# Performance work log

Hardware: AMD Instinct MI355X
Metric: run time of the kernel (lower is better)

Reference implementation:

```python
import jax, jax.numpy as jnp
import numpy as np

EPS = 1e-6

def _phi(x):
    # ELU + 1 feature map: strictly positive
    return jax.nn.elu(x) + 1.0

def setup_inputs() -> dict:
    key = jax.random.key(0)
    kq, kk, kv = jax.random.split(key, 3)
    B, T, H, D = 4, 8192, 16, 64
    q = jax.random.normal(kq, (B, T, H, D), dtype=jnp.float32)
    k = jax.random.normal(kk, (B, T, H, D), dtype=jnp.float32)
    v = jax.random.normal(kv, (B, T, H, D), dtype=jnp.float32)
    return {"q": q, "k": k, "v": v}

def _linear_attention(q, k, v):
    # q,k,v: [B,T,H,D] -> out [B,T,H,D]
    phi_q = _phi(q)
    phi_k = _phi(k)
    # time-major for scan: [T,B,H,D]
    pq = jnp.moveaxis(phi_q, 1, 0)
    pk = jnp.moveaxis(phi_k, 1, 0)
    vv = jnp.moveaxis(v, 1, 0)
    B, H, D = pq.shape[1], pq.shape[2], pq.shape[3]
    S0 = jnp.zeros((B, H, D, D), dtype=q.dtype)
    z0 = jnp.zeros((B, H, D), dtype=q.dtype)

    def step(carry, inp):
        S, z = carry
        q_t, k_t, v_t = inp  # each [B,H,D]
        S = S + k_t[..., :, None] * v_t[..., None, :]  # [B,H,D,D]
        z = z + k_t
        num = jnp.einsum('bhd,bhde->bhe', q_t, S)
        den = jnp.einsum('bhd,bhd->bh', q_t, z) + EPS
        return (S, z), num / den[..., None]

    _, out = jax.lax.scan(step, (S0, z0), (pq, pk, vv))
    return jnp.moveaxis(out, 0, 1)  # [B,T,H,D]

def reference(q, k, v):
    return _linear_attention(q, k, v)
```

## Files before the change

kernel.cpp:

```cpp
#include <hip/hip_runtime.h>
#include <hip/hip_bf16.h>


#define EPS_ 1e-6f

constexpr int Bc  = 4;
constexpr int Tc  = 8192;
constexpr int Hc  = 16;
constexpr int Dc  = 64;
constexpr int CH  = 128;
constexpr int NCH = Tc / CH;
constexpr int BHc = Bc * Hc;
constexpr int REC = Dc * Dc + Dc;
constexpr int SEG = 16;
constexpr int CPS = NCH / SEG;

typedef short  bf16x8 __attribute__((ext_vector_type(8)));
typedef float  f32x4  __attribute__((ext_vector_type(4)));

__device__ __forceinline__ float phi_f(float x) {
    return x > 0.f ? x + 1.f : __expf(x);
}
__device__ __forceinline__ unsigned short f2b(float x) {
    __hip_bfloat16 b = __float2bfloat16(x);
    return __builtin_bit_cast(unsigned short, b);
}
__device__ __forceinline__ float b2f(unsigned short u) {
    return __uint_as_float(((unsigned)u) << 16);
}

__global__ __launch_bounds__(256, 4) void k_chunkscan(const float* __restrict__ kin,
                                                      const float* __restrict__ vin,
                                                      float* __restrict__ ws) {
    const int blk = blockIdx.x;
    const int bh  = blk >> 4, seg = blk & (SEG - 1);
    const int b   = bh >> 4,  h   = bh & 15;
    const int tid = threadIdx.x;
    const int w = tid >> 6, lane = tid & 63;
    const int l15 = lane & 15, quad = lane >> 4;

    __shared__ unsigned short ktr[64][136];
    __shared__ unsigned short vtr[64][136];
    __shared__ float zred[16][64];

    const int c0 = (tid & 15) << 2;
    const int rl = (tid >> 4) << 2;

    f32x4 acc[4];
    #pragma unroll
    for (int nt = 0; nt < 4; nt++) acc[nt] = (f32x4){0.f, 0.f, 0.f, 0.f};
    float zrun = 0.f;

    for (int i = 0; i < CPS; ++i) {
        const int c  = seg * CPS + i;
        const int t0 = c * CH;

        unsigned short hk[2][4][4], hv[2][4][4];
        float zp[4] = {0.f, 0.f, 0.f, 0.f};
        #pragma unroll
        for (int sh = 0; sh < 2; ++sh) {
            const int r0 = rl + sh * 64;
            #pragma unroll
            for (int jj = 0; jj < 4; ++jj) {
                const size_t g = ((((size_t)b * Tc) + (t0 + r0 + jj)) * Hc + h) * Dc + c0;
                const float4 kk = *(const float4*)(kin + g);
                const float4 vv = *(const float4*)(vin + g);
                hk[sh][jj][0] = f2b(phi_f(kk.x)); hk[sh][jj][1] = f2b(phi_f(kk.y));
                hk[sh][jj][2] = f2b(phi_f(kk.z)); hk[sh][jj][3] = f2b(phi_f(kk.w));
                hv[sh][jj][0] = f2b(vv.x); hv[sh][jj][1] = f2b(vv.y);
                hv[sh][jj][2] = f2b(vv.z); hv[sh][jj][3] = f2b(vv.w);
                #pragma unroll
                for (int j = 0; j < 4; ++j) zp[j] += b2f(hk[sh][jj][j]);
            }
        }
        __syncthreads();

        #pragma unroll
        for (int sh = 0; sh < 2; ++sh) {
            const int r0 = rl + sh * 64;
            #pragma unroll
            for (int j = 0; j < 4; ++j) {
                *(ushort4*)&ktr[c0 + j][r0] =
                    make_ushort4(hk[sh][0][j], hk[sh][1][j], hk[sh][2][j], hk[sh][3][j]);
                *(ushort4*)&vtr[c0 + j][r0] =
                    make_ushort4(hv[sh][0][j], hv[sh][1][j], hv[sh][2][j], hv[sh][3][j]);
            }
        }
        #pragma unroll
        for (int j = 0; j < 4; ++j) zred[tid >> 4][c0 + j] = zp[j];

        float* rec = ws + (size_t)(bh * NCH + c) * REC;
        if (i > 0) {
            #pragma unroll
            for (int nt = 0; nt < 4; nt++)
                #pragma unroll
                for (int r = 0; r < 4; r++)
                    rec[(16 * w + quad * 4 + r) * 64 + 16 * nt + l15] = acc[nt][r];
        }
        __syncthreads();

        if (tid < 64) {
            if (i > 0) rec[4096 + tid] = zrun;
            float zs = 0.f;
            #pragma unroll
            for (int g = 0; g < 16; g++) zs += zred[g][tid];
            zrun += zs;
        }

        #pragma unroll
        for (int ks = 0; ks < 4; ks++) {
            bf16x8 a = *(const bf16x8*)&vtr[16 * w + l15][quad * 8 + ks * 32];
            #pragma unroll
            for (int nt = 0; nt < 4; nt++) {
                bf16x8 bb = *(const bf16x8*)&ktr[16 * nt + l15][quad * 8 + ks * 32];
                acc[nt] = __builtin_amdgcn_mfma_f32_16x16x32_bf16(a, bb, acc[nt], 0, 0, 0);
            }
        }
    }

    {
        float* rec0 = ws + (size_t)(bh * NCH + seg * CPS) * REC;
        #pragma unroll
        for (int nt = 0; nt < 4; nt++)
            #pragma unroll
            for (int r = 0; r < 4; r++)
                rec0[(16 * w + quad * 4 + r) * 64 + 16 * nt + l15] = acc[nt][r];
        if (tid < 64) rec0[4096 + tid] = zrun;
    }
}

__global__ __launch_bounds__(256) void k_segscan(float* __restrict__ ws) {
    const int bh = blockIdx.x;
    const int e  = blockIdx.y * 256 + threadIdx.x;
    if (e >= REC) return;
    float* p = ws + (size_t)bh * NCH * REC + e;
    float t[SEG];
    #pragma unroll
    for (int s = 0; s < SEG; ++s) t[s] = p[(size_t)(s * CPS) * REC];
    float run = 0.f;
    #pragma unroll
    for (int s = 0; s < SEG; ++s) { p[(size_t)(s * CPS) * REC] = run; run += t[s]; }
}

__global__ __launch_bounds__(512, 4) void k_output(const float* __restrict__ qin,
                                                   const float* __restrict__ kin,
                                                   const float* __restrict__ vin,
                                                   const float* __restrict__ ws,
                                                   float* __restrict__ outp) {
    const int chunk = blockIdx.x;
    const int bh = chunk >> 6, c = chunk & (NCH - 1);
    const int b = bh >> 4, h = bh & 15;
    const int t0 = c * CH;
    const int tid = threadIdx.x;
    const int w = tid >> 6, lane = tid & 63;
    const int l15 = lane & 15, quad = lane >> 4;

    __shared__ unsigned short qb[128][72];
    __shared__ unsigned short kb[128][72];
    __shared__ unsigned short sb[64][72];
    __shared__ unsigned short vb[64][136];
    __shared__ float zsh[64];
    __shared__ float den[128];

    {
        const int row = tid >> 2, cb = (tid & 3) << 4;
        const size_t g = ((((size_t)b * Tc) + (t0 + row)) * Hc + h) * Dc + cb;
        const float4* qp = (const float4*)(qin + g);
        const float4* kp = (const float4*)(kin + g);
        #pragma unroll
        for (int i = 0; i < 4; i++) {
            float4 qq = qp[i];
            float4 kk = kp[i];
            *(ushort4*)&qb[row][cb + 4 * i] =
                make_ushort4(f2b(phi_f(qq.x)), f2b(phi_f(qq.y)), f2b(phi_f(qq.z)), f2b(phi_f(qq.w)));
            *(ushort4*)&kb[row][cb + 4 * i] =
                make_ushort4(f2b(phi_f(kk.x)), f2b(phi_f(kk.y)), f2b(phi_f(kk.z)), f2b(phi_f(kk.w)));
        }
    }
    {
        const int c0 = (tid & 15) << 2;
        const int r0 = (tid >> 4) << 2;
        unsigned short hv[4][4];
        #pragma unroll
        for (int jj = 0; jj < 4; ++jj) {
            const size_t g = ((((size_t)b * Tc) + (t0 + r0 + jj)) * Hc + h) * Dc + c0;
            const float4 vv = *(const float4*)(vin + g);
            hv[jj][0] = f2b(vv.x); hv[jj][1] = f2b(vv.y);
            hv[jj][2] = f2b(vv.z); hv[jj][3] = f2b(vv.w);
        }
        #pragma unroll
        for (int j = 0; j < 4; ++j)
            *(ushort4*)&vb[c0 + j][r0] = make_ushort4(hv[0][j], hv[1][j], hv[2][j], hv[3][j]);
    }
    {
        const float* rec = ws + (size_t)chunk * REC;
        const float* bse = ws + (size_t)(bh * NCH + (c & ~(CPS - 1))) * REC;
        const bool cz = ((c & (CPS - 1)) == 0);
        #pragma unroll
        for (int i = 0; i < 2; i++) {
            const int idx = tid + i * 512;
            float4 sv = ((const float4*)rec)[idx];
            float4 bv = ((const float4*)bse)[idx];
            float4 t;
            if (cz) t = bv;
            else { t.x = sv.x + bv.x; t.y = sv.y + bv.y; t.z = sv.z + bv.z; t.w = sv.w + bv.w; }
            const int flat = idx * 4, e = flat >> 6, d = flat & 63;
            *(ushort4*)&sb[e][d] = make_ushort4(f2b(t.x), f2b(t.y), f2b(t.z), f2b(t.w));
        }
        if (tid < 16) {
            float4 zv = ((const float4*)(rec + 4096))[tid];
            float4 bz = ((const float4*)(bse + 4096))[tid];
            float4 t;
            if (cz) t = bz;
            else { t.x = zv.x + bz.x; t.y = zv.y + bz.y; t.z = zv.z + bz.z; t.w = zv.w + bz.w; }
            zsh[tid * 4 + 0] = t.x; zsh[tid * 4 + 1] = t.y;
            zsh[tid * 4 + 2] = t.z; zsh[tid * 4 + 3] = t.w;
        }
    }
    __syncthreads();

    if (tid < 128) {
        float s = 0.f;
        #pragma unroll
        for (int j = 0; j < 8; j++) {
            bf16x8 qv = *(const bf16x8*)&qb[tid][j * 8];
            #pragma unroll
            for (int u = 0; u < 8; u++) s += b2f((unsigned short)qv[u]) * zsh[j * 8 + u];
        }
        den[tid] = s + EPS_;
    }

    f32x4 acc[4];
    #pragma unroll
    for (int nt = 0; nt < 4; nt++) acc[nt] = (f32x4){0.f, 0.f, 0.f, 0.f};
    #pragma unroll
    for (int ks = 0; ks < 2; ks++) {
        bf16x8 a = *(const bf16x8*)&qb[16 * w + l15][quad * 8 + ks * 32];
        #pragma unroll
        for (int nt = 0; nt < 4; nt++) {
            bf16x8 bb = *(const bf16x8*)&sb[16 * nt + l15][quad * 8 + ks * 32];
            acc[nt] = __builtin_amdgcn_mfma_f32_16x16x32_bf16(a, bb, acc[nt], 0, 0, 0);
        }
    }

    f32x4 wt[8];
    #pragma unroll
    for (int nt = 0; nt < 8; nt++) wt[nt] = (f32x4){0.f, 0.f, 0.f, 0.f};
    #pragma unroll
    for (int ks = 0; ks < 2; ks++) {
        bf16x8 a = *(const bf16x8*)&qb[16 * w + l15][quad * 8 + ks * 32];
        #pragma unroll
        for (int nt = 0; nt < 4; nt++) {
            bf16x8 bb = *(const bf16x8*)&kb[16 * nt + l15][quad * 8 + ks * 32];
            wt[nt] = __builtin_amdgcn_mfma_f32_16x16x32_bf16(a, bb, wt[nt], 0, 0, 0);
        }
        if (w >= 4) {
            #pragma unroll
            for (int nt = 4; nt < 8; nt++) {
                bf16x8 bb = *(const bf16x8*)&kb[16 * nt + l15][quad * 8 + ks * 32];
                wt[nt] = __builtin_amdgcn_mfma_f32_16x16x32_bf16(a, bb, wt[nt], 0, 0, 0);
            }
        }
    }
    __syncthreads();

    {
        const int tbase = 16 * w + quad * 4;
        float rsum[4] = {0.f, 0.f, 0.f, 0.f};
        #pragma unroll
        for (int nt = 0; nt < 4; nt++) {
            const int s = 16 * nt + l15;
            #pragma unroll
            for (int r = 0; r < 4; r++) {
                float val = (s > tbase + r) ? 0.f : wt[nt][r];
                unsigned short wb16 = f2b(val);
                kb[tbase + r][s] = wb16;
                rsum[r] += b2f(wb16);
            }
        }
        if (w >= 4) {
            #pragma unroll
            for (int nt = 4; nt < 8; nt++) {
                const int s = 16 * nt + l15;
                #pragma unroll
                for (int r = 0; r < 4; r++) {
                    float val = (s > tbase + r) ? 0.f : wt[nt][r];
                    unsigned short wb16 = f2b(val);
                    qb[tbase + r][s - 64] = wb16;
                    rsum[r] += b2f(wb16);
                }
            }
        }
        #pragma unroll
        for (int r = 0; r < 4; r++) {
            float rs = rsum[r];
            rs += __shfl_xor(rs, 8, 16);
            rs += __shfl_xor(rs, 4, 16);
            rs += __shfl_xor(rs, 2, 16);
            rs += __shfl_xor(rs, 1, 16);
            if (l15 == 0) den[tbase + r] += rs;
        }
    }
    __syncthreads();

    #pragma unroll
    for (int ks = 0; ks < 2; ks++) {
        bf16x8 a = *(const bf16x8*)&kb[16 * w + l15][quad * 8 + ks * 32];
        #pragma unroll
        for (int nt = 0; nt < 4; nt++) {
            bf16x8 bb = *(const bf16x8*)&vb[16 * nt + l15][quad * 8 + ks * 32];
            acc[nt] = __builtin_amdgcn_mfma_f32_16x16x32_bf16(a, bb, acc[nt], 0, 0, 0);
        }
    }
    if (w >= 4) {
        #pragma unroll
        for (int ks = 2; ks < 4; ks++) {
            bf16x8 a = *(const bf16x8*)&qb[16 * w + l15][quad * 8 + (ks - 2) * 32];
            #pragma unroll
            for (int nt = 0; nt < 4; nt++) {
                bf16x8 bb = *(const bf16x8*)&vb[16 * nt + l15][quad * 8 + ks * 32];
                acc[nt] = __builtin_amdgcn_mfma_f32_16x16x32_bf16(a, bb, acc[nt], 0, 0, 0);
            }
        }
    }

    #pragma unroll
    for (int r = 0; r < 4; r++) {
        const int t = 16 * w + quad * 4 + r;
        const float inv = 1.0f / den[t];
        const size_t gbase = ((((size_t)b * Tc) + (t0 + t)) * Hc + h) * Dc;
        #pragma unroll
        for (int nt = 0; nt < 4; nt++) {
            outp[gbase + 16 * nt + l15] = acc[nt][r] * inv;
        }
    }
}

extern "C" void kernel_launch(void* const* d_in, const int* in_sizes, int n_in,
                              void* d_out, int out_size, void* d_ws, size_t ws_size,
                              hipStream_t stream) {
    const float* q = (const float*)d_in[0];
    const float* k = (const float*)d_in[1];
    const float* v = (const float*)d_in[2];
    float* out = (float*)d_out;
    float* ws  = (float*)d_ws;

    k_chunkscan<<<BHc * SEG, 256, 0, stream>>>(k, v, ws);
    dim3 g2(BHc, (REC + 255) / 256);
    k_segscan<<<g2, 256, 0, stream>>>(ws);
    k_output<<<BHc * NCH, 512, 0, stream>>>(q, k, v, ws, out);
}
```

Baseline: 501.3 us.

## Prefetch next chunk in chunk-scan and XOR-swizzle transposed LDS tiles

The chunk-scan loop now issues global loads for the next chunk's k/v before the MFMA accumulation of the current chunk, a register-level software pipeline meant to hide memory latency. The transposed k/v tiles in shared memory (and the v tile in the output kernel) use an XOR swizzle on the column index to reduce LDS bank conflicts. The zred array is also padded. Keeping the prefetched values live raises register pressure, which could cut occupancy under launch_bounds(256,4).

```diff
diff --git a/kernel.cpp b/kernel.cpp
--- a/kernel.cpp
+++ b/kernel.cpp
@@ -28,6 +28,9 @@
 __device__ __forceinline__ float b2f(unsigned short u) {
     return __uint_as_float(((unsigned)u) << 16);
 }
+__device__ __forceinline__ int swz(int row, int colu) {
+    return row * 136 + (colu ^ (((row >> 2) & 7) << 3));
+}
 
 __global__ __launch_bounds__(256, 4) void k_chunkscan(const float* __restrict__ kin,
                                                       const float* __restrict__ vin,
@@ -39,9 +42,9 @@
     const int w = tid >> 6, lane = tid & 63;
     const int l15 = lane & 15, quad = lane >> 4;
 
-    __shared__ unsigned short ktr[64][136];
-    __shared__ unsigned short vtr[64][136];
-    __shared__ float zred[16][64];
+    __shared__ unsigned short ktr[64 * 136];
+    __shared__ unsigned short vtr[64 * 136];
+    __shared__ float zred[16][68];
 
     const int c0 = (tid & 15) << 2;
     const int rl = (tid >> 4) << 2;
@@ -51,18 +54,17 @@
     for (int nt = 0; nt < 4; nt++) acc[nt] = (f32x4){0.f, 0.f, 0.f, 0.f};
     float zrun = 0.f;
 
-    for (int i = 0; i < CPS; ++i) {
-        const int c  = seg * CPS + i;
-        const int t0 = c * CH;
-
-        unsigned short hk[2][4][4], hv[2][4][4];
-        float zp[4] = {0.f, 0.f, 0.f, 0.f};
+    unsigned short hk[2][4][4], hv[2][4][4];
+    float zp[4];
+
+    auto load_chunk = [&](int c) {
+        zp[0] = zp[1] = zp[2] = zp[3] = 0.f;
         #pragma unroll
         for (int sh = 0; sh < 2; ++sh) {
             const int r0 = rl + sh * 64;
             #pragma unroll
             for (int jj = 0; jj < 4; ++jj) {
-                const size_t g = ((((size_t)b * Tc) + (t0 + r0 + jj)) * Hc + h) * Dc + c0;
+                const size_t g = ((((size_t)b * Tc) + (c * CH + r0 + jj)) * Hc + h) * Dc + c0;
                 const float4 kk = *(const float4*)(kin + g);
                 const float4 vv = *(const float4*)(vin + g);
                 hk[sh][jj][0] = f2b(phi_f(kk.x)); hk[sh][jj][1] = f2b(phi_f(kk.y));
@@ -73,6 +75,14 @@
                 for (int j = 0; j < 4; ++j) zp[j] += b2f(hk[sh][jj][j]);
             }
         }
+    };
+
+    load_chunk(seg * CPS);
+
+    for (int i = 0; i < CPS; ++i) {
+        const int c = seg * CPS + i;
+        float* rec = ws + (size_t)(bh * NCH + c) * REC;
+
         __syncthreads();
 
         #pragma unroll
@@ -80,16 +90,15 @@
             const int r0 = rl + sh * 64;
             #pragma unroll
             for (int j = 0; j < 4; ++j) {
-                *(ushort4*)&ktr[c0 + j][r0] =
+                *(ushort4*)&ktr[swz(c0 + j, r0)] =
                     make_ushort4(hk[sh][0][j], hk[sh][1][j], hk[sh][2][j], hk[sh][3][j]);
-                *(ushort4*)&vtr[c0 + j][r0] =
+                *(ushort4*)&vtr[swz(c0 + j, r0)] =
                     make_ushort4(hv[sh][0][j], hv[sh][1][j], hv[sh][2][j], hv[sh][3][j]);
             }
         }
         #pragma unroll
         for (int j = 0; j < 4; ++j) zred[tid >> 4][c0 + j] = zp[j];
 
-        float* rec = ws + (size_t)(bh * NCH + c) * REC;
         if (i > 0) {
             #pragma unroll
             for (int nt = 0; nt < 4; nt++)
@@ -99,23 +108,25 @@
         }
         __syncthreads();
 
+        float zs = 0.f;
         if (tid < 64) {
             if (i > 0) rec[4096 + tid] = zrun;
-            float zs = 0.f;
             #pragma unroll
             for (int g = 0; g < 16; g++) zs += zred[g][tid];
-            zrun += zs;
-        }
+        }
+
+        if (i + 1 < CPS) load_chunk(c + 1);
 
         #pragma unroll
         for (int ks = 0; ks < 4; ks++) {
-            bf16x8 a = *(const bf16x8*)&vtr[16 * w + l15][quad * 8 + ks * 32];
+            bf16x8 a = *(const bf16x8*)&vtr[swz(16 * w + l15, quad * 8 + ks * 32)];
             #pragma unroll
             for (int nt = 0; nt < 4; nt++) {
-                bf16x8 bb = *(const bf16x8*)&ktr[16 * nt + l15][quad * 8 + ks * 32];
+                bf16x8 bb = *(const bf16x8*)&ktr[swz(16 * nt + l15, quad * 8 + ks * 32)];
                 acc[nt] = __builtin_amdgcn_mfma_f32_16x16x32_bf16(a, bb, acc[nt], 0, 0, 0);
             }
         }
+        if (tid < 64) zrun += zs;
     }
 
     {
@@ -158,7 +169,7 @@
     __shared__ unsigned short qb[128][72];
     __shared__ unsigned short kb[128][72];
     __shared__ unsigned short sb[64][72];
-    __shared__ unsigned short vb[64][136];
+    __shared__ unsigned short vb[64 * 136];
     __shared__ float zsh[64];
     __shared__ float den[128];
 
@@ -190,7 +201,7 @@
         }
         #pragma unroll
         for (int j = 0; j < 4; ++j)
-            *(ushort4*)&vb[c0 + j][r0] = make_ushort4(hv[0][j], hv[1][j], hv[2][j], hv[3][j]);
+            *(ushort4*)&vb[swz(c0 + j, r0)] = make_ushort4(hv[0][j], hv[1][j], hv[2][j], hv[3][j]);
     }
     {
         const float* rec = ws + (size_t)chunk * REC;
@@ -308,7 +319,7 @@
         bf16x8 a = *(const bf16x8*)&kb[16 * w + l15][quad * 8 + ks * 32];
         #pragma unroll
         for (int nt = 0; nt < 4; nt++) {
-            bf16x8 bb = *(const bf16x8*)&vb[16 * nt + l15][quad * 8 + ks * 32];
+            bf16x8 bb = *(const bf16x8*)&vb[swz(16 * nt + l15, quad * 8 + ks * 32)];
             acc[nt] = __builtin_amdgcn_mfma_f32_16x16x32_bf16(a, bb, acc[nt], 0, 0, 0);
         }
     }
@@ -318,7 +329,7 @@
             bf16x8 a = *(const bf16x8*)&qb[16 * w + l15][quad * 8 + (ks - 2) * 32];
             #pragma unroll
             for (int nt = 0; nt < 4; nt++) {
-                bf16x8 bb = *(const bf16x8*)&vb[16 * nt + l15][quad * 8 + ks * 32];
+                bf16x8 bb = *(const bf16x8*)&vb[swz(16 * nt + l15, quad * 8 + ks * 32)];
                 acc[nt] = __builtin_amdgcn_mfma_f32_16x16x32_bf16(a, bb, acc[nt], 0, 0, 0);
             }
         }
```

After: 507.6 us. Within noise of the previous version (+1.2%).
